# Performance work log

Hardware: AMD Instinct MI355X
Metric: run time of the kernel (lower is better)

The kernel has to match this reference:

```python
import jax, jax.numpy as jnp
import numpy as np

N = 200000
B = 1024          # batch_size (number of graphs/segments)
D = 256           # in_channels
STEPS = 3         # processing_steps


def setup_inputs() -> dict:
    key = jax.random.key(0)
    ks = jax.random.split(key, 6)
    x = jax.random.normal(ks[0], (N, D), dtype=jnp.float32)
    bank_kg = jnp.zeros((1,), dtype=jnp.float32)  # unused by forward
    batch = jnp.sort(jax.random.randint(ks[1], (N,), 0, B, dtype=jnp.int32))
    q_star = jax.random.normal(ks[2], (B, 2 * D), dtype=jnp.float32)
    s = 1.0 / np.sqrt(D)  # PyTorch LSTM init scale
    W_ih = jax.random.uniform(ks[3], (4 * D, 2 * D), jnp.float32, -s, s)
    W_hh = jax.random.uniform(ks[4], (4 * D, D), jnp.float32, -s, s)
    b_ih = jnp.zeros((4 * D,), dtype=jnp.float32)
    b_hh = jnp.zeros((4 * D,), dtype=jnp.float32)
    return {"x": x, "bank_kg": bank_kg, "batch": batch, "q_star": q_star,
            "W_ih": W_ih, "W_hh": W_hh, "b_ih": b_ih, "b_hh": b_hh}


def _lstm_cell(inp, h, c, W_ih, W_hh, b_ih, b_hh):
    # PyTorch gate order: i, f, g, o
    gates = inp @ W_ih.T + b_ih + h @ W_hh.T + b_hh  # [B, 4D]
    i, f, g, o = jnp.split(gates, 4, axis=-1)
    i = jax.nn.sigmoid(i)
    f = jax.nn.sigmoid(f)
    g = jnp.tanh(g)
    o = jax.nn.sigmoid(o)
    c = f * c + i * g
    h = o * jnp.tanh(c)
    return h, c


def _segment_softmax(e, batch, num_segments):
    # numerically stable softmax over nodes grouped by segment id
    emax = jax.ops.segment_max(e, batch, num_segments=num_segments)
    emax = jnp.where(jnp.isfinite(emax), emax, 0.0)  # guard empty segments
    ee = jnp.exp(e - emax[batch])
    denom = jax.ops.segment_sum(ee, batch, num_segments=num_segments)
    return ee / (denom[batch] + 1e-16)


def reference(x, bank_kg, batch, q_star, W_ih, W_hh, b_ih, b_hh):
    del bank_kg  # unused in the original forward
    h = jnp.zeros((B, D), dtype=x.dtype)
    c = jnp.zeros((B, D), dtype=x.dtype)
    for _ in range(STEPS):
        h, c = _lstm_cell(q_star, h, c, W_ih, W_hh, b_ih, b_hh)
        q = h                                       # [B, D]
        e = jnp.sum(x * q[batch], axis=-1)          # [N] attention logits
        a = _segment_softmax(e, batch, B)           # [N]
        r = jax.ops.segment_sum(a[:, None] * x, batch, num_segments=B)  # [B, D]
        q_star = jnp.concatenate([q, r], axis=-1)   # [B, 2D]
    return q_star
```

## Files before the change

### kernel.cpp

```cpp
#include <hip/hip_runtime.h>
#include <hip/hip_bf16.h>
#include <cstdint>


#define NN     200000
#define BSEG   1024
#define DD     256
#define KA     512
#define FOURD  1024

using bf16x8 = __attribute__((ext_vector_type(8))) __bf16;
using f32x4  = __attribute__((ext_vector_type(4))) float;

__device__ __forceinline__ float bf2f(unsigned int u) {
  union { unsigned int i; float f; } v; v.i = (u & 0xffffu) << 16; return v.f;
}
__device__ __forceinline__ unsigned short f2bf(float f) {
  union { float f; unsigned int i; } v; v.f = f;
  unsigned int x = v.i;
  if ((x & 0x7fffffffu) > 0x7f800000u) return (unsigned short)((x >> 16) | 0x40);
  return (unsigned short)((x + 0x7fffu + ((x >> 16) & 1u)) >> 16);
}
__device__ __forceinline__ void split_bf(float f, unsigned short& hi, unsigned short& lo) {
  hi = f2bf(f);
  lo = f2bf(f - bf2f(hi));
}

__global__ void prep_all(const int* __restrict__ batch, int* __restrict__ segs,
                         const float* __restrict__ Wih, const float* __restrict__ Whh,
                         const float* __restrict__ bih, const float* __restrict__ bhh,
                         unsigned short* __restrict__ W1hi, unsigned short* __restrict__ W1lo,
                         unsigned short* __restrict__ W2hi, unsigned short* __restrict__ W2lo,
                         float* __restrict__ bias,
                         const float* __restrict__ qst,
                         unsigned short* __restrict__ Ahi, unsigned short* __restrict__ Alo,
                         float* __restrict__ c) {
  int idx = blockIdx.x * 256 + threadIdx.x;
  if (idx <= BSEG) {
    int lo = 0, hi = NN;
    while (lo < hi) { int mid = (lo + hi) >> 1; if (batch[mid] < idx) lo = mid + 1; else hi = mid; }
    segs[idx] = lo;
  }
  if (idx < FOURD) bias[idx] = bih[idx] + bhh[idx];
  if (idx < FOURD * KA) {
    int j = idx / KA, k = idx - j * KA;
    float w1 = Wih[j * 512 + k];
    float w2 = (k < 256) ? (Wih[j * 512 + k] + Whh[j * 256 + k])
                         : Wih[j * 512 + k];
    unsigned short hi, lo;
    split_bf(w1, hi, lo); W1hi[idx] = hi; W1lo[idx] = lo;
    split_bf(w2, hi, lo); W2hi[idx] = hi; W2lo[idx] = lo;
  }
  if (idx < BSEG * KA) {
    unsigned short hi, lo; split_bf(qst[idx], hi, lo);
    Ahi[idx] = hi; Alo[idx] = lo;
  }
  if (idx < BSEG * DD) c[idx] = 0.f;
}

__global__ __launch_bounds__(256) void gemm_gates(const unsigned short* __restrict__ Ahi,
                                                  const unsigned short* __restrict__ Alo,
                                                  const unsigned short* __restrict__ Whi,
                                                  const unsigned short* __restrict__ Wlo,
                                                  float* __restrict__ gates) {
  int bx = blockIdx.x;
  int m0 = (bx >> 5) << 7;
  int n0 = (bx & 31) << 5;
  int t = threadIdx.x, w = t >> 6, lane = t & 63;
  int r16 = lane & 15, quad = lane >> 4;

  __shared__ unsigned short sWhi[32 * 64];
  __shared__ unsigned short sWlo[32 * 64];

  f32x4 acc[2][2] = {};

  const unsigned short* a0h = Ahi + (size_t)(m0 + 32 * w + r16) * KA + quad * 8;
  const unsigned short* a0l = Alo + (size_t)(m0 + 32 * w + r16) * KA + quad * 8;

  int srow = t >> 3;
  int scb  = t & 7;
  const unsigned short* gwh = Whi + (size_t)(n0 + srow) * KA + scb * 8;
  const unsigned short* gwl = Wlo + (size_t)(n0 + srow) * KA + scb * 8;
  int sdst = srow * 64 + ((scb ^ (srow & 7)) * 8);

  for (int kc = 0; kc < KA; kc += 64) {
    __syncthreads();
    *(bf16x8*)&sWhi[sdst] = *(const bf16x8*)(gwh + kc);
    *(bf16x8*)&sWlo[sdst] = *(const bf16x8*)(gwl + kc);
    __syncthreads();
    #pragma unroll
    for (int ks = 0; ks < 2; ++ks) {
      bf16x8 bh[2], bl[2];
      #pragma unroll
      for (int ni = 0; ni < 2; ++ni) {
        int wr = 16 * ni + r16;
        int off = wr * 64 + (((ks * 4 + quad) ^ (wr & 7)) * 8);
        bh[ni] = *(const bf16x8*)&sWhi[off];
        bl[ni] = *(const bf16x8*)&sWlo[off];
      }
      #pragma unroll
      for (int ms = 0; ms < 2; ++ms) {
        bf16x8 a  = *(const bf16x8*)(a0h + (size_t)ms * 16 * KA + kc + ks * 32);
        bf16x8 al = *(const bf16x8*)(a0l + (size_t)ms * 16 * KA + kc + ks * 32);
        #pragma unroll
        for (int ni = 0; ni < 2; ++ni) {
          acc[ms][ni] = __builtin_amdgcn_mfma_f32_16x16x32_bf16(a,  bh[ni], acc[ms][ni], 0, 0, 0);
          acc[ms][ni] = __builtin_amdgcn_mfma_f32_16x16x32_bf16(a,  bl[ni], acc[ms][ni], 0, 0, 0);
          acc[ms][ni] = __builtin_amdgcn_mfma_f32_16x16x32_bf16(al, bh[ni], acc[ms][ni], 0, 0, 0);
        }
      }
    }
  }
  #pragma unroll
  for (int ms = 0; ms < 2; ++ms)
    #pragma unroll
    for (int ni = 0; ni < 2; ++ni)
      #pragma unroll
      for (int r = 0; r < 4; ++r)
        gates[(size_t)(m0 + 32 * w + 16 * ms + quad * 4 + r) * FOURD
              + n0 + 16 * ni + r16] = acc[ms][ni][r];
}

__global__ __launch_bounds__(256) void attn_fused(const float* __restrict__ x,
                                                  const int* __restrict__ segs,
                                                  const float* __restrict__ gates,
                                                  const float* __restrict__ bias,
                                                  float* __restrict__ c,
                                                  unsigned short* __restrict__ Ahi,
                                                  unsigned short* __restrict__ Alo,
                                                  float* __restrict__ qout) {
  int b = blockIdx.x, t = threadIdx.x;
  int w = t >> 6, lane = t & 63;

  const float* g = gates + (size_t)b * FOURD;
  float gi = g[t]       + bias[t];
  float gf = g[256 + t] + bias[256 + t];
  float gg = g[512 + t] + bias[512 + t];
  float go = g[768 + t] + bias[768 + t];
  float ig = 1.f / (1.f + expf(-gi));
  float fg = 1.f / (1.f + expf(-gf));
  float gt = tanhf(gg);
  float og = 1.f / (1.f + expf(-go));
  int cidx = b * DD + t;
  float cn = fg * c[cidx] + ig * gt;
  c[cidx] = cn;
  float hn = og * tanhf(cn);

  __shared__ __align__(16) float sh[DD];
  sh[t] = hn;
  {
    unsigned short hi, lo; split_bf(hn, hi, lo);
    size_t ro = (size_t)b * KA;
    Ahi[ro + t] = hi;  Alo[ro + t] = lo;
    qout[(size_t)b * 512 + t] = hn;
  }
  __syncthreads();

  int s = segs[b], tend = segs[b + 1];
  float4 q = *(const float4*)(sh + lane * 4);

  float m = -3.402823466e38f;
  float l = 0.f;
  float4 v = {0.f, 0.f, 0.f, 0.f};

  int i = s + w;
  float4 xv = {0.f, 0.f, 0.f, 0.f};
  if (i < tend) xv = *(const float4*)(x + (size_t)i * DD + lane * 4);
  for (; i < tend; i += 4) {
    float4 cur = xv;
    int nx = i + 4;
    if (nx < tend) xv = *(const float4*)(x + (size_t)nx * DD + lane * 4);
    float d = cur.x * q.x + cur.y * q.y + cur.z * q.z + cur.w * q.w;
    #pragma unroll
    for (int off = 32; off; off >>= 1) d += __shfl_xor(d, off);
    float mn = fmaxf(m, d);
    float alpha = __expf(m - mn);
    float wgt   = __expf(d - mn);
    l = l * alpha + wgt;
    v.x = v.x * alpha + wgt * cur.x;
    v.y = v.y * alpha + wgt * cur.y;
    v.z = v.z * alpha + wgt * cur.z;
    v.w = v.w * alpha + wgt * cur.w;
    m = mn;
  }

  __shared__ float sm[4], sl[4];
  __shared__ __align__(16) float sv[4][DD];
  if (lane == 0) { sm[w] = m; sl[w] = l; }
  *(float4*)(&sv[w][lane * 4]) = v;
  __syncthreads();

  float M = fmaxf(fmaxf(sm[0], sm[1]), fmaxf(sm[2], sm[3]));
  if (M < -1e37f) M = 0.f;
  float a0 = __expf(sm[0] - M), a1 = __expf(sm[1] - M);
  float a2 = __expf(sm[2] - M), a3 = __expf(sm[3] - M);
  float L = sl[0] * a0 + sl[1] * a1 + sl[2] * a2 + sl[3] * a3;
  float r = (sv[0][t] * a0 + sv[1][t] * a1 + sv[2][t] * a2 + sv[3][t] * a3)
            / (L + 1e-16f);

  unsigned short hi, lo; split_bf(r, hi, lo);
  size_t ro = (size_t)b * KA;
  Ahi[ro + DD + t] = hi;  Alo[ro + DD + t] = lo;
  qout[(size_t)b * 512 + DD + t] = r;
}

extern "C" void kernel_launch(void* const* d_in, const int* in_sizes, int n_in,
                              void* d_out, int out_size, void* d_ws, size_t ws_size,
                              hipStream_t stream) {
  const float* x    = (const float*)d_in[0];
  const int*   batc = (const int*)d_in[2];
  const float* qst  = (const float*)d_in[3];
  const float* Wih  = (const float*)d_in[4];
  const float* Whh  = (const float*)d_in[5];
  const float* bih  = (const float*)d_in[6];
  const float* bhh  = (const float*)d_in[7];
  float* out = (float*)d_out;

  char* ws = (char*)d_ws;
  size_t off = 0;
  auto alloc = [&](size_t bytes) -> void* {
    void* p = ws + off; off = (off + bytes + 255) & ~(size_t)255; return p;
  };
  int*            segs = (int*)alloc((size_t)(BSEG + 1) * 4);
  unsigned short* W1hi = (unsigned short*)alloc((size_t)FOURD * KA * 2);
  unsigned short* W1lo = (unsigned short*)alloc((size_t)FOURD * KA * 2);
  unsigned short* W2hi = (unsigned short*)alloc((size_t)FOURD * KA * 2);
  unsigned short* W2lo = (unsigned short*)alloc((size_t)FOURD * KA * 2);
  unsigned short* Ahi  = (unsigned short*)alloc((size_t)BSEG * KA * 2);
  unsigned short* Alo  = (unsigned short*)alloc((size_t)BSEG * KA * 2);
  float*          gate = (float*)alloc((size_t)BSEG * FOURD * 4);
  float*          c    = (float*)alloc((size_t)BSEG * DD * 4);
  float*          bias = (float*)alloc((size_t)FOURD * 4);

  prep_all<<<(FOURD * KA + 255) / 256, 256, 0, stream>>>(
      batc, segs, Wih, Whh, bih, bhh, W1hi, W1lo, W2hi, W2lo, bias, qst, Ahi, Alo, c);

  for (int step = 0; step < 3; ++step) {
    const unsigned short* whi = step ? W2hi : W1hi;
    const unsigned short* wlo = step ? W2lo : W1lo;
    gemm_gates<<<256, 256, 0, stream>>>(Ahi, Alo, whi, wlo, gate);
    attn_fused<<<BSEG, 256, 0, stream>>>(x, segs, gate, bias, c, Ahi, Alo, out);
  }
}
```

Before: 425.2 us.

## Process four rows per wave iteration with triple-buffered prefetch in attention

Each wave now handles blocks of four consecutive rows per step and keeps three such blocks of loads in flight, replacing the single-row, single-prefetch loop. The four dot-product reductions are interleaved and the online softmax is updated once per four rows, so fewer serial max/exp rescales are needed. This targets memory latency in a pass that is bound by streaming x. The cost is more registers per thread, and the clamped duplicate loads at segment tails cause redundant reads.

```diff
diff --git a/kernel.cpp b/kernel.cpp
--- a/kernel.cpp
+++ b/kernel.cpp
@@ -121,6 +121,45 @@
               + n0 + 16 * ni + r16] = acc[ms][ni][r];
 }
 
+
+#define LDG(buf, base) do {                                                 \
+    int r0_ = (base);                                                       \
+    int r1_ = (base) + 1 < tend ? (base) + 1 : tend - 1;                    \
+    int r2_ = (base) + 2 < tend ? (base) + 2 : tend - 1;                    \
+    int r3_ = (base) + 3 < tend ? (base) + 3 : tend - 1;                    \
+    buf[0] = *(const float4*)(x + (size_t)r0_ * DD + lane * 4);             \
+    buf[1] = *(const float4*)(x + (size_t)r1_ * DD + lane * 4);             \
+    buf[2] = *(const float4*)(x + (size_t)r2_ * DD + lane * 4);             \
+    buf[3] = *(const float4*)(x + (size_t)r3_ * DD + lane * 4);             \
+  } while (0)
+
+#define PROC(buf, base) do {                                                \
+    float dx_ = buf[0].x*q.x + buf[0].y*q.y + buf[0].z*q.z + buf[0].w*q.w;  \
+    float dy_ = buf[1].x*q.x + buf[1].y*q.y + buf[1].z*q.z + buf[1].w*q.w;  \
+    float dz_ = buf[2].x*q.x + buf[2].y*q.y + buf[2].z*q.z + buf[2].w*q.w;  \
+    float dw_ = buf[3].x*q.x + buf[3].y*q.y + buf[3].z*q.z + buf[3].w*q.w;  \
+    _Pragma("unroll")                                                       \
+    for (int off_ = 32; off_; off_ >>= 1) {                                 \
+      dx_ += __shfl_xor(dx_, off_);                                         \
+      dy_ += __shfl_xor(dy_, off_);                                         \
+      dz_ += __shfl_xor(dz_, off_);                                         \
+      dw_ += __shfl_xor(dw_, off_);                                         \
+    }                                                                       \
+    if ((base) + 1 >= tend) dy_ = -3.402823466e38f;                         \
+    if ((base) + 2 >= tend) dz_ = -3.402823466e38f;                         \
+    if ((base) + 3 >= tend) dw_ = -3.402823466e38f;                         \
+    float mn_ = fmaxf(fmaxf(fmaxf(dx_, dy_), fmaxf(dz_, dw_)), m);          \
+    float al_ = __expf(m - mn_);                                            \
+    float w0_ = __expf(dx_ - mn_), w1_ = __expf(dy_ - mn_);                 \
+    float w2_ = __expf(dz_ - mn_), w3_ = __expf(dw_ - mn_);                 \
+    l = l * al_ + (w0_ + w1_) + (w2_ + w3_);                                \
+    v.x = (v.x*al_ + w0_*buf[0].x) + (w1_*buf[1].x + w2_*buf[2].x) + w3_*buf[3].x; \
+    v.y = (v.y*al_ + w0_*buf[0].y) + (w1_*buf[1].y + w2_*buf[2].y) + w3_*buf[3].y; \
+    v.z = (v.z*al_ + w0_*buf[0].z) + (w1_*buf[1].z + w2_*buf[2].z) + w3_*buf[3].z; \
+    v.w = (v.w*al_ + w0_*buf[0].w) + (w1_*buf[1].w + w2_*buf[2].w) + w3_*buf[3].w; \
+    m = mn_;                                                                \
+  } while (0)
+
 __global__ __launch_bounds__(256) void attn_fused(const float* __restrict__ x,
                                                   const int* __restrict__ segs,
                                                   const float* __restrict__ gates,
@@ -163,25 +202,22 @@
   float l = 0.f;
   float4 v = {0.f, 0.f, 0.f, 0.f};
 
-  int i = s + w;
-  float4 xv = {0.f, 0.f, 0.f, 0.f};
-  if (i < tend) xv = *(const float4*)(x + (size_t)i * DD + lane * 4);
-  for (; i < tend; i += 4) {
-    float4 cur = xv;
-    int nx = i + 4;
-    if (nx < tend) xv = *(const float4*)(x + (size_t)nx * DD + lane * 4);
-    float d = cur.x * q.x + cur.y * q.y + cur.z * q.z + cur.w * q.w;
-    #pragma unroll
-    for (int off = 32; off; off >>= 1) d += __shfl_xor(d, off);
-    float mn = fmaxf(m, d);
-    float alpha = __expf(m - mn);
-    float wgt   = __expf(d - mn);
-    l = l * alpha + wgt;
-    v.x = v.x * alpha + wgt * cur.x;
-    v.y = v.y * alpha + wgt * cur.y;
-    v.z = v.z * alpha + wgt * cur.z;
-    v.w = v.w * alpha + wgt * cur.w;
-    m = mn;
+  int i0 = s + w * 4;
+  float4 b0[4], b1[4], b2[4];
+  if (i0      < tend) LDG(b0, i0);
+  if (i0 + 16 < tend) LDG(b1, i0 + 16);
+  if (i0 + 32 < tend) LDG(b2, i0 + 32);
+  for (int i = i0; i < tend; i += 48) {
+    PROC(b0, i);
+    if (i + 48 < tend) LDG(b0, i + 48);
+    if (i + 16 < tend) {
+      PROC(b1, i + 16);
+      if (i + 64 < tend) LDG(b1, i + 64);
+      if (i + 32 < tend) {
+        PROC(b2, i + 32);
+        if (i + 80 < tend) LDG(b2, i + 80);
+      }
+    }
   }
 
   __shared__ float sm[4], sl[4];
```

Measured after the change: 423.9 us. No clear change (-0.3%).

## Tile attention rows through swizzled LDS in 32-row blocks with block-wide softmax

Applied to the files above, without the earlier changes.

Replaces the per-row wave-level online softmax with a tiled scheme. Each block stages 32 rows of x into XOR-swizzled shared memory and prefetches the next tile into registers. Logits are computed with 8 lanes per row, reducing shuffle depth, and the running max is rescaled once per tile instead of once per row. This cuts the serial shuffle-and-exp chain per row, at the cost of two extra barriers per tile, about 37KB of shared memory, and the extra register file needed for the prefetch. It also adds an occupancy hint to the launch bounds.

```diff
diff --git a/kernel.cpp b/kernel.cpp
--- a/kernel.cpp
+++ b/kernel.cpp
@@ -121,14 +121,14 @@
               + n0 + 16 * ni + r16] = acc[ms][ni][r];
 }
 
-__global__ __launch_bounds__(256) void attn_fused(const float* __restrict__ x,
-                                                  const int* __restrict__ segs,
-                                                  const float* __restrict__ gates,
-                                                  const float* __restrict__ bias,
-                                                  float* __restrict__ c,
-                                                  unsigned short* __restrict__ Ahi,
-                                                  unsigned short* __restrict__ Alo,
-                                                  float* __restrict__ qout) {
+__global__ __launch_bounds__(256, 4) void attn_fused(const float* __restrict__ x,
+                                                     const int* __restrict__ segs,
+                                                     const float* __restrict__ gates,
+                                                     const float* __restrict__ bias,
+                                                     float* __restrict__ c,
+                                                     unsigned short* __restrict__ Ahi,
+                                                     unsigned short* __restrict__ Alo,
+                                                     float* __restrict__ qout) {
   int b = blockIdx.x, t = threadIdx.x;
   int w = t >> 6, lane = t & 63;
 
@@ -146,8 +146,13 @@
   c[cidx] = cn;
   float hn = og * tanhf(cn);
 
-  __shared__ __align__(16) float sh[DD];
-  sh[t] = hn;
+  __shared__ float shq[DD];
+  __shared__ __align__(16) float xt[32 * DD];
+  __shared__ float se[32];
+  __shared__ float sm[4], sl[4];
+  __shared__ __align__(16) float sv[4][DD];
+
+  shq[t ^ (4 * ((t >> 5) & 7))] = hn;
   {
     unsigned short hi, lo; split_bf(hn, hi, lo);
     size_t ro = (size_t)b * KA;
@@ -156,36 +161,78 @@
   }
   __syncthreads();
 
-  int s = segs[b], tend = segs[b + 1];
-  float4 q = *(const float4*)(sh + lane * 4);
-
-  float m = -3.402823466e38f;
-  float l = 0.f;
+  int s = segs[b], e = segs[b + 1];
+  int r8 = lane >> 3, d8 = lane & 7;
+
+  float m = -3.402823466e38f, l = 0.f;
   float4 v = {0.f, 0.f, 0.f, 0.f};
 
-  int i = s + w;
-  float4 xv = {0.f, 0.f, 0.f, 0.f};
-  if (i < tend) xv = *(const float4*)(x + (size_t)i * DD + lane * 4);
-  for (; i < tend; i += 4) {
-    float4 cur = xv;
-    int nx = i + 4;
-    if (nx < tend) xv = *(const float4*)(x + (size_t)nx * DD + lane * 4);
-    float d = cur.x * q.x + cur.y * q.y + cur.z * q.z + cur.w * q.w;
-    #pragma unroll
-    for (int off = 32; off; off >>= 1) d += __shfl_xor(d, off);
-    float mn = fmaxf(m, d);
+  int R = e - s; if (R > 32) R = 32;
+  float4 st[8];
+  #pragma unroll
+  for (int k = 0; k < 8; ++k) {
+    int i = w + 4 * k;
+    if (i < R) st[k] = *(const float4*)(x + (size_t)(s + i) * DD + lane * 4);
+  }
+
+  for (int tb = s; tb < e; tb += 32) {
+    __syncthreads();
+    #pragma unroll
+    for (int k = 0; k < 8; ++k) {
+      int i = w + 4 * k;
+      if (i < R) *(float4*)&xt[i * DD + ((4 * lane) ^ (4 * (i & 7)))] = st[k];
+    }
+    __syncthreads();
+
+    int Rn = e - (tb + 32); if (Rn > 32) Rn = 32;
+    #pragma unroll
+    for (int k = 0; k < 8; ++k) {
+      int i = w + 4 * k;
+      if (i < Rn) st[k] = *(const float4*)(x + (size_t)(tb + 32 + i) * DD + lane * 4);
+    }
+
+    {
+      int i = 8 * w + r8;
+      int key = 4 * (i & 7);
+      float4 acc = {0.f, 0.f, 0.f, 0.f};
+      #pragma unroll
+      for (int cc = 0; cc < 8; ++cc) {
+        int j = d8 * 32 + 4 * cc;
+        float4 xv = *(const float4*)&xt[i * DD + (j ^ key)];
+        float4 qv = *(const float4*)&shq[j ^ (4 * d8)];
+        acc.x += xv.x * qv.x; acc.y += xv.y * qv.y;
+        acc.z += xv.z * qv.z; acc.w += xv.w * qv.w;
+      }
+      float ee = (acc.x + acc.y) + (acc.z + acc.w);
+      ee += __shfl_xor(ee, 1);
+      ee += __shfl_xor(ee, 2);
+      ee += __shfl_xor(ee, 4);
+      if (i >= R) ee = -3.402823466e38f;
+      if (d8 == 0) se[i] = ee;
+    }
+    __syncthreads();
+
+    float tm = se[lane & 31];
+    #pragma unroll
+    for (int mask = 16; mask; mask >>= 1) tm = fmaxf(tm, __shfl_xor(tm, mask));
+    float mn = fmaxf(m, tm);
     float alpha = __expf(m - mn);
-    float wgt   = __expf(d - mn);
-    l = l * alpha + wgt;
-    v.x = v.x * alpha + wgt * cur.x;
-    v.y = v.y * alpha + wgt * cur.y;
-    v.z = v.z * alpha + wgt * cur.z;
-    v.w = v.w * alpha + wgt * cur.w;
+    l *= alpha; v.x *= alpha; v.y *= alpha; v.z *= alpha; v.w *= alpha;
+
+    #pragma unroll
+    for (int k = 0; k < 8; ++k) {
+      int i = w + 4 * k;
+      if (i < R) {
+        float wv = __expf(se[i] - mn);
+        float4 xv = *(const float4*)&xt[i * DD + ((4 * lane) ^ (4 * (i & 7)))];
+        l += wv;
+        v.x += wv * xv.x; v.y += wv * xv.y; v.z += wv * xv.z; v.w += wv * xv.w;
+      }
+    }
     m = mn;
-  }
-
-  __shared__ float sm[4], sl[4];
-  __shared__ __align__(16) float sv[4][DD];
+    R = Rn;
+  }
+
   if (lane == 0) { sm[w] = m; sl[w] = l; }
   *(float4*)(&sv[w][lane * 4]) = v;
   __syncthreads();
```

Result: slower. 637.6 us (+49.9%).
